# Optimization experiments

Hardware: AMD Instinct MI355X
Metric: run time of the kernel (lower is better)

Reference implementation:

```python
import jax, jax.numpy as jnp
import numpy as np

BN_EPS = 1e-5


def setup_inputs() -> dict:
    key = jax.random.key(0)
    ks = jax.random.split(key, 8)
    B, C, H, W = 8, 256, 64, 64
    Cqk = C // 8  # query/key channels = out_channels // 8
    x = jax.random.normal(ks[0], (B, C, H, W), dtype=jnp.float32)
    # 1x1 convs == per-pixel matmuls; kaiming-normal-ish scale
    wq = jax.random.normal(ks[1], (Cqk, C), dtype=jnp.float32) * np.sqrt(2.0 / C)
    bq = jnp.zeros((Cqk,), dtype=jnp.float32)
    wk = jax.random.normal(ks[2], (Cqk, C), dtype=jnp.float32) * np.sqrt(2.0 / C)
    bk = jnp.zeros((Cqk,), dtype=jnp.float32)
    wv = jax.random.normal(ks[3], (C, C), dtype=jnp.float32) * np.sqrt(2.0 / C)
    bv = jnp.zeros((C,), dtype=jnp.float32)
    # gamma is initialized to 0 in the original; use a small nonzero value so
    # the attention path actually contributes (and has nontrivial gradients)
    gamma = jnp.full((1,), 0.5, dtype=jnp.float32)
    bn_weight = jnp.ones((C,), dtype=jnp.float32)
    bn_bias = jnp.zeros((C,), dtype=jnp.float32)
    return {"x": x, "wq": wq, "bq": bq, "wk": wk, "bk": bk,
            "wv": wv, "bv": bv, "gamma": gamma,
            "bn_weight": bn_weight, "bn_bias": bn_bias}


def reference(x, wq, bq, wk, bk, wv, bv, gamma, bn_weight, bn_bias):
    B, C, H, W = x.shape
    N = H * W
    xf = x.reshape(B, C, N)  # (B, C, N)
    # 1x1 conv projections as channel matmuls
    q = jnp.einsum('oc,bcn->bno', wq, xf) + bq            # (B, N, Cqk)
    k = jnp.einsum('oc,bcn->bon', wk, xf) + bk[:, None]   # (B, Cqk, N)
    v = jnp.einsum('oc,bcn->bon', wv, xf) + bv[:, None]   # (B, C, N)
    # attention[b, i, j] = softmax_j(q_i . k_j)  -- full N x N matrix
    scores = jnp.einsum('bno,bom->bnm', q, k)             # (B, N, N)
    attn = jax.nn.softmax(scores, axis=2)
    # out[b, c, i] = sum_j v[b, c, j] * attn[b, i, j]
    out = jnp.einsum('bcj,bij->bci', v, attn)             # (B, C, N)
    out = out.reshape(B, C, H, W)
    out = gamma[0] * out + x
    # BatchNorm2d in training mode: batch statistics over (B, H, W)
    mean = jnp.mean(out, axis=(0, 2, 3), keepdims=True)
    var = jnp.var(out, axis=(0, 2, 3), keepdims=True)
    out = (out - mean) * jax.lax.rsqrt(var + BN_EPS)
    out = out * bn_weight[None, :, None, None] + bn_bias[None, :, None, None]
    return jax.nn.relu(out)
```

## Files before the change

kernel.cpp:

```cpp
#include <hip/hip_runtime.h>
#include <stdint.h>

#define B_ 8
#define C_ 256
#define N_ 4096
#define CQK 32

typedef __attribute__((ext_vector_type(8))) _Float16 f16x8;
typedef __attribute__((ext_vector_type(4))) float f32x4;

__device__ __forceinline__ unsigned short f2bf_rne(float f) {
  unsigned u = __builtin_bit_cast(unsigned, f);
  u += 0x7FFFu + ((u >> 16) & 1u);
  return (unsigned short)(u >> 16);
}

__global__ __launch_bounds__(256) void xpose_kernel(
    const float* __restrict__ x, _Float16* __restrict__ xT)
{
  __shared__ float xs[64 * 129];
  const int t  = threadIdx.x;
  const int blk = blockIdx.x;
  const int nt = blk & 31;
  const int ct = (blk >> 5) & 3;
  const int b  = blk >> 7;
  const int c0 = ct * 64, n0 = nt * 128;

  #pragma unroll
  for (int p = 0; p < 8; ++p) {
    int cc = p * 8 + (t >> 5);
    int nn = (t & 31) * 4;
    float4 v = *(const float4*)(x + ((size_t)(b * C_ + c0 + cc)) * N_ + n0 + nn);
    xs[cc * 129 + nn]     = v.x;
    xs[cc * 129 + nn + 1] = v.y;
    xs[cc * 129 + nn + 2] = v.z;
    xs[cc * 129 + nn + 3] = v.w;
  }
  __syncthreads();
  #pragma unroll
  for (int p = 0; p < 4; ++p) {
    int id = p * 256 + t;
    int cchunk = id & 7, n = id >> 3;
    _Float16 h[8];
    #pragma unroll
    for (int j = 0; j < 8; ++j) h[j] = (_Float16)xs[(cchunk * 8 + j) * 129 + n];
    *(f16x8*)(xT + ((size_t)(b * N_) + n0 + n) * C_ + c0 + cchunk * 8) = *(f16x8*)h;
  }
}

__global__ __launch_bounds__(256) void wconv_kernel(
    const float* __restrict__ wq, const float* __restrict__ wk,
    const float* __restrict__ wv, _Float16* __restrict__ wf)
{
  int idx = blockIdx.x * 256 + threadIdx.x;
  int e = idx * 4;
  int o = e >> 8, c = e & 255;
  const float* src;
  if (o < 32)      src = wq + o * 256 + c;
  else if (o < 64) src = wk + (o - 32) * 256 + c;
  else             src = wv + (o - 64) * 256 + c;
  float4 v = *(const float4*)src;
  _Float16 h[4] = {(_Float16)v.x, (_Float16)v.y, (_Float16)v.z, (_Float16)v.w};
  *(uint2*)(wf + e) = *(uint2*)h;
}

__global__ __launch_bounds__(256, 4) void proj_gemm_kernel(
    const _Float16* __restrict__ xT, const _Float16* __restrict__ wf,
    const float* __restrict__ bq, const float* __restrict__ bk,
    const float* __restrict__ bv,
    _Float16* __restrict__ qf, _Float16* __restrict__ kf,
    _Float16* __restrict__ vout)
{
  const int t = threadIdx.x, lane = t & 63;
  const int w = t >> 6;
  const int l15 = lane & 15, q4 = lane >> 4;
  const int blk = blockIdx.x;
  const int otile = blk % 5;
  const int nt = blk / 5;
  const int b  = nt >> 5;
  const int n0 = (nt & 31) * 128;
  const int o0w = (w & 1) * 32;
  const int n0w = (w >> 1) * 64;

  f32x4 acc[2][4];
  const f32x4 zf = {0.f, 0.f, 0.f, 0.f};
  #pragma unroll
  for (int a = 0; a < 2; ++a)
    #pragma unroll
    for (int bb = 0; bb < 4; ++bb) acc[a][bb] = zf;

  const _Float16* wbase = wf + (size_t)(otile * 64 + o0w) * 256;
  const _Float16* xbase = xT + ((size_t)(b * N_) + n0 + n0w) * C_;

  #pragma unroll
  for (int kc = 0; kc < 8; ++kc) {
    f16x8 af[2], bfr[4];
    #pragma unroll
    for (int ob = 0; ob < 2; ++ob)
      af[ob] = *(const f16x8*)(wbase + (ob * 16 + l15) * 256 + kc * 32 + q4 * 8);
    #pragma unroll
    for (int nb = 0; nb < 4; ++nb)
      bfr[nb] = *(const f16x8*)(xbase + (nb * 16 + l15) * 256 + kc * 32 + q4 * 8);
    #pragma unroll
    for (int ob = 0; ob < 2; ++ob)
      #pragma unroll
      for (int nb = 0; nb < 4; ++nb)
        acc[ob][nb] = __builtin_amdgcn_mfma_f32_16x16x32_f16(af[ob], bfr[nb], acc[ob][nb], 0, 0, 0);
  }

  if (otile == 0) {
    _Float16* dst = (o0w == 0) ? qf : kf;
    const float* bias = (o0w == 0) ? bq : bk;
    #pragma unroll
    for (int ob = 0; ob < 2; ++ob) {
      float4 b4 = *(const float4*)(bias + ob * 16 + q4 * 4);
      #pragma unroll
      for (int nb = 0; nb < 4; ++nb) {
        int pixel = n0 + n0w + nb * 16 + l15;
        _Float16 h[4];
        h[0] = (_Float16)(acc[ob][nb][0] + b4.x);
        h[1] = (_Float16)(acc[ob][nb][1] + b4.y);
        h[2] = (_Float16)(acc[ob][nb][2] + b4.z);
        h[3] = (_Float16)(acc[ob][nb][3] + b4.w);
        *(uint2*)(dst + ((size_t)(b * N_) + pixel) * CQK + ob * 16 + q4 * 4) = *(uint2*)h;
      }
    }
  } else {
    int cbase = (otile - 1) * 64 + o0w;
    #pragma unroll
    for (int ob = 0; ob < 2; ++ob) {
      float4 b4 = *(const float4*)(bv + cbase + ob * 16 + q4 * 4);
      #pragma unroll
      for (int nb = 0; nb < 4; ++nb) {
        int pixel = n0 + n0w + nb * 16 + l15;
        #pragma unroll
        for (int r = 0; r < 4; ++r) {
          int c = cbase + ob * 16 + q4 * 4 + r;
          float bval = (r == 0) ? b4.x : (r == 1) ? b4.y : (r == 2) ? b4.z : b4.w;
          vout[((size_t)(b * C_) + c) * N_ + pixel] = (_Float16)(acc[ob][nb][r] + bval);
        }
      }
    }
  }
}

__global__ __launch_bounds__(512, 4) void attn_kernel(
    const float* __restrict__ x, const float* __restrict__ gptr,
    const _Float16* __restrict__ qf, const _Float16* __restrict__ kf,
    const _Float16* __restrict__ vf, unsigned short* __restrict__ yout)
{
  __shared__ __align__(16) char smem[10768];
  _Float16* Plds  = (_Float16*)smem;
  float* pmax   = (float*)(smem + 9216);
  float* psum   = (float*)(smem + 9728);
  float* alphal = (float*)(smem + 10240);
  float* lrowl  = (float*)(smem + 10496);
  int*   flagl  = (int*)(smem + 10752);

  const int t = threadIdx.x, lane = t & 63;
  const int w = t >> 6;
  const int l15 = lane & 15, q4 = lane >> 4;
  const int b  = blockIdx.x & 7;
  const int it = blockIdx.x >> 3;
  const int i0 = it * 64;
  const int qg = w >> 1, jh = w & 1;
  const int row = qg * 16 + l15;
  const float gamma = gptr[0];

  const f16x8 qfr = *(const f16x8*)(qf + ((size_t)(b * N_) + i0 + qg * 16 + l15) * CQK + q4 * 8);

  f32x4 acc[2][4];
  const f32x4 zf = {0.f, 0.f, 0.f, 0.f};
  #pragma unroll
  for (int a = 0; a < 2; ++a)
    #pragma unroll
    for (int bb = 0; bb < 4; ++bb) acc[a][bb] = zf;

  float mold = -1e30f, lrun = 0.f;

  for (int jt = 0; jt < N_ / 64; ++jt) {
    const int jbase = jt * 64;

    f16x8 kfr[2];
    #pragma unroll
    for (int jbb = 0; jbb < 2; ++jbb) {
      int j = jbase + (jh * 2 + jbb) * 16 + l15;
      kfr[jbb] = *(const f16x8*)(kf + ((size_t)(b * N_) + j) * CQK + q4 * 8);
    }
    f16x8 vfr[2][2];
    #pragma unroll
    for (int ks = 0; ks < 2; ++ks)
      #pragma unroll
      for (int cb = 0; cb < 2; ++cb)
        vfr[ks][cb] = *(const f16x8*)(vf + ((size_t)(b * C_) + w * 32 + cb * 16 + l15) * N_ + jbase + ks * 32 + q4 * 8);

    f32x4 sv[2];
    #pragma unroll
    for (int jbb = 0; jbb < 2; ++jbb)
      sv[jbb] = __builtin_amdgcn_mfma_f32_16x16x32_f16(kfr[jbb], qfr, zf, 0, 0, 0);

    float lm = fmaxf(fmaxf(fmaxf(sv[0][0], sv[0][1]), fmaxf(sv[0][2], sv[0][3])),
                     fmaxf(fmaxf(sv[1][0], sv[1][1]), fmaxf(sv[1][2], sv[1][3])));
    lm = fmaxf(lm, __shfl_xor(lm, 16));
    lm = fmaxf(lm, __shfl_xor(lm, 32));
    if (lane < 16) pmax[jh * 64 + qg * 16 + lane] = lm;
    __syncthreads();

    float mnew = fmaxf(mold, fmaxf(pmax[row], pmax[64 + row]));
    bool upd = mnew > mold;
    float alpha = __expf(mold - mnew);
    float p[2][4];
    float ts = 0.f;
    #pragma unroll
    for (int jbb = 0; jbb < 2; ++jbb)
      #pragma unroll
      for (int r = 0; r < 4; ++r) {
        float pv = __expf(sv[jbb][r] - mnew);
        p[jbb][r] = pv; ts += pv;
      }
    ts += __shfl_xor(ts, 16);
    ts += __shfl_xor(ts, 32);
    if (lane < 16) psum[jh * 64 + qg * 16 + lane] = ts;
    if (jh == 0 && lane < 16) alphal[qg * 16 + lane] = alpha;
    {
      char* pb = (char*)Plds + (qg * 16 + l15) * 144 + jh * 64 + q4 * 8;
      #pragma unroll
      for (int jbb = 0; jbb < 2; ++jbb) {
        _Float16 h[4];
        h[0] = (_Float16)p[jbb][0];
        h[1] = (_Float16)p[jbb][1];
        h[2] = (_Float16)p[jbb][2];
        h[3] = (_Float16)p[jbb][3];
        *(uint2*)(pb + jbb * 32) = *(uint2*)h;
      }
    }
    if (__ballot(upd) != 0ull) { if (lane == 0) flagl[jt & 1] = 1; }
    if (t == 0) flagl[(jt + 1) & 1] = 0;
    mold = mnew;
    __syncthreads();

    lrun = lrun * alpha + psum[row] + psum[64 + row];

    if (flagl[jt & 1]) {
      #pragma unroll
      for (int ib = 0; ib < 4; ++ib) {
        float av = alphal[ib * 16 + l15];
        #pragma unroll
        for (int cb = 0; cb < 2; ++cb)
          #pragma unroll
          for (int r = 0; r < 4; ++r) acc[cb][ib][r] *= av;
      }
    }
    #pragma unroll
    for (int ks = 0; ks < 2; ++ks) {
      f16x8 pf[4];
      #pragma unroll
      for (int ib = 0; ib < 4; ++ib)
        pf[ib] = *(const f16x8*)((char*)Plds + (ib * 16 + l15) * 144 + ks * 64 + q4 * 16);
      #pragma unroll
      for (int cb = 0; cb < 2; ++cb)
        #pragma unroll
        for (int ib = 0; ib < 4; ++ib)
          acc[cb][ib] = __builtin_amdgcn_mfma_f32_16x16x32_f16(vfr[ks][cb], pf[ib], acc[cb][ib], 0, 0, 0);
    }
  }

  if (jh == 0 && lane < 16) lrowl[qg * 16 + lane] = lrun;
  __syncthreads();
  #pragma unroll
  for (int ib = 0; ib < 4; ++ib) {
    float linv = 1.0f / lrowl[ib * 16 + l15];
    int i = i0 + ib * 16 + l15;
    #pragma unroll
    for (int cb = 0; cb < 2; ++cb) {
      #pragma unroll
      for (int r = 0; r < 4; ++r) {
        int c = w * 32 + cb * 16 + q4 * 4 + r;
        size_t off = ((size_t)(b * C_) + c) * N_ + i;
        float o = acc[cb][ib][r] * linv;
        yout[off] = f2bf_rne(fmaf(gamma, o, x[off]));
      }
    }
  }
}

__global__ __launch_bounds__(256) void bnstats_kernel(
    const unsigned short* __restrict__ y, float* __restrict__ meanw, float* __restrict__ rstdw)
{
  const int c = blockIdx.x;
  const int t = threadIdx.x;
  float s1 = 0.f, s2 = 0.f;
  for (int b = 0; b < B_; ++b) {
    const unsigned short* p = y + ((size_t)(b * C_ + c)) * N_;
    #pragma unroll
    for (int r = 0; r < 2; ++r) {
      uint4 u = *(const uint4*)(p + r * 2048 + t * 8);
      unsigned uu[4] = {u.x, u.y, u.z, u.w};
      #pragma unroll
      for (int k = 0; k < 4; ++k) {
        float a = __builtin_bit_cast(float, uu[k] << 16);
        float bb = __builtin_bit_cast(float, uu[k] & 0xFFFF0000u);
        s1 += a + bb;
        s2 += a * a + bb * bb;
      }
    }
  }
  __shared__ float r1[256], r2[256];
  r1[t] = s1; r2[t] = s2;
  __syncthreads();
  for (int s = 128; s > 0; s >>= 1) {
    if (t < s) { r1[t] += r1[t + s]; r2[t] += r2[t + s]; }
    __syncthreads();
  }
  if (t == 0) {
    float mean = r1[0] * (1.0f / 32768.0f);
    float var  = r2[0] * (1.0f / 32768.0f) - mean * mean;
    meanw[c] = mean;
    rstdw[c] = rsqrtf(var + 1e-5f);
  }
}

__global__ __launch_bounds__(256) void bnapply_kernel(
    const unsigned short* __restrict__ y, float* __restrict__ out,
    const float* __restrict__ meanw, const float* __restrict__ rstdw,
    const float* __restrict__ bnw, const float* __restrict__ bnb)
{
  size_t idx = (size_t)blockIdx.x * 256 + threadIdx.x;
  size_t el = idx * 8;
  int c = (int)((el >> 12) & 255);
  float sc = bnw[c] * rstdw[c];
  float sh = fmaf(-meanw[c], sc, bnb[c]);
  uint4 u = *(const uint4*)(y + el);
  unsigned uu[4] = {u.x, u.y, u.z, u.w};
  float4 o0, o1;
  float v[8];
  #pragma unroll
  for (int k = 0; k < 4; ++k) {
    v[2 * k]     = __builtin_bit_cast(float, uu[k] << 16);
    v[2 * k + 1] = __builtin_bit_cast(float, uu[k] & 0xFFFF0000u);
  }
  o0.x = fmaxf(fmaf(v[0], sc, sh), 0.f);
  o0.y = fmaxf(fmaf(v[1], sc, sh), 0.f);
  o0.z = fmaxf(fmaf(v[2], sc, sh), 0.f);
  o0.w = fmaxf(fmaf(v[3], sc, sh), 0.f);
  o1.x = fmaxf(fmaf(v[4], sc, sh), 0.f);
  o1.y = fmaxf(fmaf(v[5], sc, sh), 0.f);
  o1.z = fmaxf(fmaf(v[6], sc, sh), 0.f);
  o1.w = fmaxf(fmaf(v[7], sc, sh), 0.f);
  *(float4*)(out + el) = o0;
  *(float4*)(out + el + 4) = o1;
}

extern "C" void kernel_launch(void* const* d_in, const int* in_sizes, int n_in,
                              void* d_out, int out_size, void* d_ws, size_t ws_size,
                              hipStream_t stream)
{
  const float* x   = (const float*)d_in[0];
  const float* wq  = (const float*)d_in[1];
  const float* bq  = (const float*)d_in[2];
  const float* wk  = (const float*)d_in[3];
  const float* bk  = (const float*)d_in[4];
  const float* wv  = (const float*)d_in[5];
  const float* bv  = (const float*)d_in[6];
  const float* gm  = (const float*)d_in[7];
  const float* bnw = (const float*)d_in[8];
  const float* bnb = (const float*)d_in[9];
  float* out = (float*)d_out;

  _Float16* xT  = (_Float16*)d_out;
  _Float16* vfp = (_Float16*)((char*)d_out + (size_t)B_ * C_ * N_ * 2);

  char* ws = (char*)d_ws;
  _Float16* qf = (_Float16*)(ws);
  _Float16* kf = (_Float16*)(ws + ((size_t)2 << 20));
  unsigned short* yout = (unsigned short*)(ws + ((size_t)4 << 20));
  _Float16* wf = (_Float16*)(ws + ((size_t)21 << 20));
  float* meanw = (float*)(ws + ((size_t)22 << 20));
  float* rstdw = (float*)(ws + ((size_t)22 << 20) + 4096);

  hipLaunchKernelGGL(xpose_kernel, dim3(1024), dim3(256), 0, stream, x, xT);
  hipLaunchKernelGGL(wconv_kernel, dim3(80), dim3(256), 0, stream, wq, wk, wv, wf);
  hipLaunchKernelGGL(proj_gemm_kernel, dim3(1280), dim3(256), 0, stream,
                     xT, wf, bq, bk, bv, qf, kf, vfp);
  hipLaunchKernelGGL(attn_kernel, dim3(512), dim3(512), 0, stream,
                     x, gm, qf, kf, vfp, yout);
  hipLaunchKernelGGL(bnstats_kernel, dim3(256), dim3(256), 0, stream,
                     yout, meanw, rstdw);
  hipLaunchKernelGGL(bnapply_kernel, dim3(4096), dim3(256), 0, stream,
                     yout, out, meanw, rstdw, bnw, bnb);
}
```

Baseline: 298.3 us.

## Restructure attention loop: per-wave full key tiles, lazy rescale, double-buffered P

Reworks the attention kernel so that each of 4 waves owns 16 query rows across the full 64-key tile and 64 output channels. This removes the cross-wave max/sum exchange and one barrier per tile. The log2(e) factor is folded into q at projection time so the kernel can use exp2f. A lazy max update (rescale only when the max grows by more than 8) skips most accumulator rescales. The P buffer and alpha values are double-buffered in LDS, K fragments are prefetched one tile ahead, and the loop is manually unrolled by two with setprio around the MFMAs. In exchange, accumulators double per wave (more register pressure, launch bounds 256,2), and the lazy rescale allows fp16 P values up to 2^8, which adds a small overflow/precision risk.

```diff
diff --git a/kernel.cpp b/kernel.cpp
--- a/kernel.cpp
+++ b/kernel.cpp
@@ -111,6 +111,7 @@
   if (otile == 0) {
     _Float16* dst = (o0w == 0) ? qf : kf;
     const float* bias = (o0w == 0) ? bq : bk;
+    const float qsc = (o0w == 0) ? 1.4426950408889634f : 1.0f;
     #pragma unroll
     for (int ob = 0; ob < 2; ++ob) {
       float4 b4 = *(const float4*)(bias + ob * 16 + q4 * 4);
@@ -118,10 +119,10 @@
       for (int nb = 0; nb < 4; ++nb) {
         int pixel = n0 + n0w + nb * 16 + l15;
         _Float16 h[4];
-        h[0] = (_Float16)(acc[ob][nb][0] + b4.x);
-        h[1] = (_Float16)(acc[ob][nb][1] + b4.y);
-        h[2] = (_Float16)(acc[ob][nb][2] + b4.z);
-        h[3] = (_Float16)(acc[ob][nb][3] + b4.w);
+        h[0] = (_Float16)((acc[ob][nb][0] + b4.x) * qsc);
+        h[1] = (_Float16)((acc[ob][nb][1] + b4.y) * qsc);
+        h[2] = (_Float16)((acc[ob][nb][2] + b4.z) * qsc);
+        h[3] = (_Float16)((acc[ob][nb][3] + b4.w) * qsc);
         *(uint2*)(dst + ((size_t)(b * N_) + pixel) * CQK + ob * 16 + q4 * 4) = *(uint2*)h;
       }
     }
@@ -144,18 +145,90 @@
   }
 }
 
-__global__ __launch_bounds__(512, 4) void attn_kernel(
+#define ATTN_BODY(JT, KC, KN) do { \
+  const int buf_ = (JT) & 1; \
+   \
+  f16x8 vv_[8]; \
+  _Pragma("unroll") \
+  for (int ks = 0; ks < 2; ++ks) { \
+    vv_[ks * 4 + 0] = *(const f16x8*)(vp0 + ks * 32); \
+    vv_[ks * 4 + 1] = *(const f16x8*)(vp1 + ks * 32); \
+    vv_[ks * 4 + 2] = *(const f16x8*)(vp2 + ks * 32); \
+    vv_[ks * 4 + 3] = *(const f16x8*)(vp3 + ks * 32); \
+  } \
+  vp0 += 64; vp1 += 64; vp2 += 64; vp3 += 64; \
+   \
+  { const _Float16* knp_ = kbase + (size_t)((((JT) + 1) & 63) * 64) * CQK; \
+    _Pragma("unroll") \
+    for (int jb = 0; jb < 4; ++jb) KN[jb] = *(const f16x8*)(knp_ + jb * 16 * CQK); } \
+   \
+  f32x4 sv_[4]; \
+  _Pragma("unroll") \
+  for (int jb = 0; jb < 4; ++jb) \
+    sv_[jb] = __builtin_amdgcn_mfma_f32_16x16x32_f16(KC[jb], qfr, zf, 0, 0, 0); \
+  float lm_ = sv_[0][0]; \
+  _Pragma("unroll") \
+  for (int jb = 0; jb < 4; ++jb) \
+    lm_ = fmaxf(lm_, fmaxf(fmaxf(sv_[jb][0], sv_[jb][1]), fmaxf(sv_[jb][2], sv_[jb][3]))); \
+  lm_ = fmaxf(lm_, __shfl_xor(lm_, 16)); \
+  lm_ = fmaxf(lm_, __shfl_xor(lm_, 32)); \
+  bool upd_ = lm_ > mold + 8.0f; \
+  unsigned long long bal_ = __ballot(upd_);             \
+  float alpha_ = upd_ ? exp2f(mold - lm_) : 1.0f; \
+  if (upd_) mold = lm_; \
+  float ts_ = 0.f; \
+  float p_[4][4]; \
+  _Pragma("unroll") \
+  for (int jb = 0; jb < 4; ++jb) \
+    _Pragma("unroll") \
+    for (int r = 0; r < 4; ++r) { p_[jb][r] = exp2f(sv_[jb][r] - mold); ts_ += p_[jb][r]; } \
+  ts_ += __shfl_xor(ts_, 16); \
+  ts_ += __shfl_xor(ts_, 32); \
+  lrun = lrun * alpha_ + ts_; \
+  { char* pb_ = (char*)Plds + buf_ * 9216 + (w * 16 + l15) * 144 + q4 * 8; \
+    _Pragma("unroll") \
+    for (int jb = 0; jb < 4; ++jb) { \
+      _Float16 h_[4] = {(_Float16)p_[jb][0], (_Float16)p_[jb][1], \
+                        (_Float16)p_[jb][2], (_Float16)p_[jb][3]}; \
+      *(uint2*)(pb_ + jb * 32) = *(uint2*)h_; } } \
+  if (q4 == 0) alphal[buf_ * 64 + w * 16 + l15] = alpha_; \
+  if (lane == 0) flagw[buf_ * 4 + w] = (bal_ != 0ull) ? 1 : 0; \
+  __syncthreads(); \
+  { int4 fl_ = *(const int4*)(flagw + buf_ * 4); \
+    if (fl_.x | fl_.y | fl_.z | fl_.w) { \
+      _Pragma("unroll") \
+      for (int ib = 0; ib < 4; ++ib) { \
+        float av_ = alphal[buf_ * 64 + ib * 16 + l15]; \
+        _Pragma("unroll") \
+        for (int cb = 0; cb < 4; ++cb) \
+          _Pragma("unroll") \
+          for (int r = 0; r < 4; ++r) acc[cb][ib][r] *= av_; } } } \
+  __builtin_amdgcn_s_setprio(1); \
+  _Pragma("unroll") \
+  for (int ks = 0; ks < 2; ++ks) { \
+    f16x8 pf_[4]; \
+    _Pragma("unroll") \
+    for (int ib = 0; ib < 4; ++ib) \
+      pf_[ib] = *(const f16x8*)((char*)Plds + buf_ * 9216 + (ib * 16 + l15) * 144 + ks * 64 + q4 * 16); \
+    _Pragma("unroll") \
+    for (int cb = 0; cb < 4; ++cb) \
+      _Pragma("unroll") \
+      for (int ib = 0; ib < 4; ++ib) \
+        acc[cb][ib] = __builtin_amdgcn_mfma_f32_16x16x32_f16(vv_[ks * 4 + cb], pf_[ib], acc[cb][ib], 0, 0, 0); \
+  } \
+  __builtin_amdgcn_s_setprio(0); \
+} while (0)
+
+__global__ __launch_bounds__(256, 2) void attn_kernel(
     const float* __restrict__ x, const float* __restrict__ gptr,
     const _Float16* __restrict__ qf, const _Float16* __restrict__ kf,
     const _Float16* __restrict__ vf, unsigned short* __restrict__ yout)
 {
-  __shared__ __align__(16) char smem[10768];
+  __shared__ __align__(16) char smem[19232];
   _Float16* Plds  = (_Float16*)smem;
-  float* pmax   = (float*)(smem + 9216);
-  float* psum   = (float*)(smem + 9728);
-  float* alphal = (float*)(smem + 10240);
-  float* lrowl  = (float*)(smem + 10496);
-  int*   flagl  = (int*)(smem + 10752);
+  float* alphal = (float*)(smem + 18432);
+  int*   flagw  = (int*)(smem + 18944);
+  float* lrowl  = (float*)(smem + 18976);
 
   const int t = threadIdx.x, lane = t & 63;
   const int w = t >> 6;
@@ -163,119 +236,46 @@
   const int b  = blockIdx.x & 7;
   const int it = blockIdx.x >> 3;
   const int i0 = it * 64;
-  const int qg = w >> 1, jh = w & 1;
-  const int row = qg * 16 + l15;
   const float gamma = gptr[0];
 
-  const f16x8 qfr = *(const f16x8*)(qf + ((size_t)(b * N_) + i0 + qg * 16 + l15) * CQK + q4 * 8);
-
-  f32x4 acc[2][4];
+  const f16x8 qfr = *(const f16x8*)(qf + ((size_t)(b * N_) + i0 + w * 16 + l15) * CQK + q4 * 8);
+
+  const _Float16* kbase = kf + ((size_t)(b * N_) + l15) * CQK + q4 * 8;
+  const _Float16* vp0 = vf + ((size_t)(b * C_) + w * 64 + l15) * N_ + q4 * 8;
+  const _Float16* vp1 = vp0 + (size_t)16 * N_;
+  const _Float16* vp2 = vp0 + (size_t)32 * N_;
+  const _Float16* vp3 = vp0 + (size_t)48 * N_;
+
+  f32x4 acc[4][4];
   const f32x4 zf = {0.f, 0.f, 0.f, 0.f};
   #pragma unroll
-  for (int a = 0; a < 2; ++a)
+  for (int a = 0; a < 4; ++a)
     #pragma unroll
     for (int bb = 0; bb < 4; ++bb) acc[a][bb] = zf;
 
   float mold = -1e30f, lrun = 0.f;
 
-  for (int jt = 0; jt < N_ / 64; ++jt) {
-    const int jbase = jt * 64;
-
-    f16x8 kfr[2];
-    #pragma unroll
-    for (int jbb = 0; jbb < 2; ++jbb) {
-      int j = jbase + (jh * 2 + jbb) * 16 + l15;
-      kfr[jbb] = *(const f16x8*)(kf + ((size_t)(b * N_) + j) * CQK + q4 * 8);
-    }
-    f16x8 vfr[2][2];
-    #pragma unroll
-    for (int ks = 0; ks < 2; ++ks)
-      #pragma unroll
-      for (int cb = 0; cb < 2; ++cb)
-        vfr[ks][cb] = *(const f16x8*)(vf + ((size_t)(b * C_) + w * 32 + cb * 16 + l15) * N_ + jbase + ks * 32 + q4 * 8);
-
-    f32x4 sv[2];
-    #pragma unroll
-    for (int jbb = 0; jbb < 2; ++jbb)
-      sv[jbb] = __builtin_amdgcn_mfma_f32_16x16x32_f16(kfr[jbb], qfr, zf, 0, 0, 0);
-
-    float lm = fmaxf(fmaxf(fmaxf(sv[0][0], sv[0][1]), fmaxf(sv[0][2], sv[0][3])),
-                     fmaxf(fmaxf(sv[1][0], sv[1][1]), fmaxf(sv[1][2], sv[1][3])));
-    lm = fmaxf(lm, __shfl_xor(lm, 16));
-    lm = fmaxf(lm, __shfl_xor(lm, 32));
-    if (lane < 16) pmax[jh * 64 + qg * 16 + lane] = lm;
-    __syncthreads();
-
-    float mnew = fmaxf(mold, fmaxf(pmax[row], pmax[64 + row]));
-    bool upd = mnew > mold;
-    float alpha = __expf(mold - mnew);
-    float p[2][4];
-    float ts = 0.f;
-    #pragma unroll
-    for (int jbb = 0; jbb < 2; ++jbb)
-      #pragma unroll
-      for (int r = 0; r < 4; ++r) {
-        float pv = __expf(sv[jbb][r] - mnew);
-        p[jbb][r] = pv; ts += pv;
-      }
-    ts += __shfl_xor(ts, 16);
-    ts += __shfl_xor(ts, 32);
-    if (lane < 16) psum[jh * 64 + qg * 16 + lane] = ts;
-    if (jh == 0 && lane < 16) alphal[qg * 16 + lane] = alpha;
-    {
-      char* pb = (char*)Plds + (qg * 16 + l15) * 144 + jh * 64 + q4 * 8;
-      #pragma unroll
-      for (int jbb = 0; jbb < 2; ++jbb) {
-        _Float16 h[4];
-        h[0] = (_Float16)p[jbb][0];
-        h[1] = (_Float16)p[jbb][1];
-        h[2] = (_Float16)p[jbb][2];
-        h[3] = (_Float16)p[jbb][3];
-        *(uint2*)(pb + jbb * 32) = *(uint2*)h;
-      }
-    }
-    if (__ballot(upd) != 0ull) { if (lane == 0) flagl[jt & 1] = 1; }
-    if (t == 0) flagl[(jt + 1) & 1] = 0;
-    mold = mnew;
-    __syncthreads();
-
-    lrun = lrun * alpha + psum[row] + psum[64 + row];
-
-    if (flagl[jt & 1]) {
-      #pragma unroll
-      for (int ib = 0; ib < 4; ++ib) {
-        float av = alphal[ib * 16 + l15];
-        #pragma unroll
-        for (int cb = 0; cb < 2; ++cb)
-          #pragma unroll
-          for (int r = 0; r < 4; ++r) acc[cb][ib][r] *= av;
-      }
-    }
-    #pragma unroll
-    for (int ks = 0; ks < 2; ++ks) {
-      f16x8 pf[4];
-      #pragma unroll
-      for (int ib = 0; ib < 4; ++ib)
-        pf[ib] = *(const f16x8*)((char*)Plds + (ib * 16 + l15) * 144 + ks * 64 + q4 * 16);
-      #pragma unroll
-      for (int cb = 0; cb < 2; ++cb)
-        #pragma unroll
-        for (int ib = 0; ib < 4; ++ib)
-          acc[cb][ib] = __builtin_amdgcn_mfma_f32_16x16x32_f16(vfr[ks][cb], pf[ib], acc[cb][ib], 0, 0, 0);
-    }
-  }
-
-  if (jh == 0 && lane < 16) lrowl[qg * 16 + lane] = lrun;
+  f16x8 ka[4], kb[4];
+  #pragma unroll
+  for (int jb = 0; jb < 4; ++jb) ka[jb] = *(const f16x8*)(kbase + jb * 16 * CQK);
+
+  #pragma unroll 1
+  for (int jt = 0; jt < 64; jt += 2) {
+    ATTN_BODY(jt, ka, kb);
+    ATTN_BODY(jt + 1, kb, ka);
+  }
+
+  if (q4 == 0) lrowl[w * 16 + l15] = lrun;
   __syncthreads();
   #pragma unroll
   for (int ib = 0; ib < 4; ++ib) {
     float linv = 1.0f / lrowl[ib * 16 + l15];
     int i = i0 + ib * 16 + l15;
     #pragma unroll
-    for (int cb = 0; cb < 2; ++cb) {
+    for (int cb = 0; cb < 4; ++cb) {
       #pragma unroll
       for (int r = 0; r < 4; ++r) {
-        int c = w * 32 + cb * 16 + q4 * 4 + r;
+        int c = w * 64 + cb * 16 + q4 * 4 + r;
         size_t off = ((size_t)(b * C_) + c) * N_ + i;
         float o = acc[cb][ib][r] * linv;
         yout[off] = f2bf_rne(fmaf(gamma, o, x[off]));
@@ -382,7 +382,7 @@
   hipLaunchKernelGGL(wconv_kernel, dim3(80), dim3(256), 0, stream, wq, wk, wv, wf);
   hipLaunchKernelGGL(proj_gemm_kernel, dim3(1280), dim3(256), 0, stream,
                      xT, wf, bq, bk, bv, qf, kf, vfp);
-  hipLaunchKernelGGL(attn_kernel, dim3(512), dim3(512), 0, stream,
+  hipLaunchKernelGGL(attn_kernel, dim3(512), dim3(256), 0, stream,
                      x, gm, qf, kf, vfp, yout);
   hipLaunchKernelGGL(bnstats_kernel, dim3(256), dim3(256), 0, stream,
                      yout, meanw, rstdw);
```

Measured after the change: 302.4 us. Within noise of the previous version (+1.4%).
